# Kernel tuning notes

Hardware: AMD Instinct MI355X
Metric: run time of the kernel (lower is better)

The kernel has to match this reference:

```python
import jax, jax.numpy as jnp
import numpy as np

B, S, D, H = 4, 2048, 1024, 16
HD = D // H  # 64


def setup_inputs() -> dict:
    key = jax.random.key(0)
    k1, k2, k3 = jax.random.split(key, 3)
    scale = 1.0 / np.sqrt(D)
    return {
        "x": jax.random.normal(k1, (B, S, D), dtype=jnp.float32),
        "W_qkv": jax.random.normal(k2, (3 * D, D), dtype=jnp.float32) * scale,
        "b_qkv": jnp.zeros((3 * D,), dtype=jnp.float32),
        "W_out": jax.random.normal(k3, (D, D), dtype=jnp.float32) * scale,
        "b_out": jnp.zeros((D,), dtype=jnp.float32),
    }


def reference(x, W_qkv, b_qkv, W_out, b_out):
    b, s, d = x.shape
    # fused QKV projection: [b, s, 3d]
    qkv = jnp.einsum("bsd,ed->bse", x, W_qkv) + b_qkv
    # [b, s, H, 3*hd] -> [b, H, s, 3*hd]
    qkv = qkv.reshape(b, s, H, 3 * HD).transpose(0, 2, 1, 3)
    q, k, v = jnp.split(qkv, 3, axis=-1)  # each [b, H, s, hd]
    scaled = jnp.einsum("bhqd,bhkd->bhqk", q, k) / jnp.sqrt(jnp.float32(HD))
    attention = jax.nn.softmax(scaled, axis=-1)  # [b, H, s, s]
    values = jnp.einsum("bhqk,bhkd->bhqd", attention, v)
    values = values.transpose(0, 2, 1, 3).reshape(b, s, d)
    out = jnp.einsum("bsd,ed->bse", values, W_out) + b_out
    return out
```

## Files before the change

### kernel.cpp

```cpp
#include <hip/hip_runtime.h>

#define SEQ   2048
#define DM    1024
#define NHEAD 16
#define NBAT  4
#define NQKV  3072
#define MTOT  8192

typedef __attribute__((ext_vector_type(8))) short bf16x8;
typedef __attribute__((ext_vector_type(4))) float f32x4;
typedef __attribute__((ext_vector_type(16))) float f32x16;

__device__ __forceinline__ unsigned short f2bf(float f) {
    union { float f; unsigned int u; } v; v.f = f;
    return (unsigned short)((v.u + 0x7FFFu + ((v.u >> 16) & 1u)) >> 16);
}

__device__ __forceinline__ void gl_lds16(const void* g, void* l) {
    __builtin_amdgcn_global_load_lds(
        (const __attribute__((address_space(1))) unsigned int*)(unsigned long long)g,
        (__attribute__((address_space(3))) unsigned int*)(unsigned int)(unsigned long long)l,
        16, 0, 0);
}

__global__ __launch_bounds__(256) void k_cvt(const float* __restrict__ src,
                                             unsigned short* __restrict__ dst, int n4) {
    int i = blockIdx.x * blockDim.x + threadIdx.x;
    if (i >= n4) return;
    float4 v = reinterpret_cast<const float4*>(src)[i];
    ushort4 o = { f2bf(v.x), f2bf(v.y), f2bf(v.z), f2bf(v.w) };
    reinterpret_cast<ushort4*>(dst)[i] = o;
}

__global__ __launch_bounds__(256) void k_qkv(const unsigned short* __restrict__ X,
                                             const unsigned short* __restrict__ W,
                                             const float* __restrict__ bias,
                                             unsigned short* __restrict__ Qb,
                                             unsigned short* __restrict__ Kb,
                                             unsigned short* __restrict__ Vtb) {
    __shared__ short As[2][128 * 32];
    __shared__ short Bs[2][128 * 32];

    const int tid = threadIdx.x;
    const int lane = tid & 63;
    const int wid = tid >> 6;
    const int lr = lane & 15, g = lane >> 4;
    const int bm = blockIdx.x / (NQKV / 128);
    const int bn = blockIdx.x % (NQKV / 128);
    const int m0 = bm * 128, n0 = bn * 128;
    const int wr = (wid >> 1) * 64, wc = (wid & 1) * 64;

    const f32x4 fz = {0.f, 0.f, 0.f, 0.f};
    f32x4 acc[4][4];
#pragma unroll
    for (int i = 0; i < 4; ++i)
#pragma unroll
        for (int j = 0; j < 4; ++j) acc[i][j] = fz;

    auto stage = [&](int buf, int kt) {
#pragma unroll
        for (int p = 0; p < 2; ++p) {
            int c = wid * 128 + p * 64 + lane;
            int r_ = c >> 2;
            int kc = (c & 3) ^ (r_ & 3);
            gl_lds16(X + (size_t)(m0 + r_) * DM + kt * 32 + kc * 8, &As[buf][c * 8]);
            gl_lds16(W + (size_t)(n0 + r_) * DM + kt * 32 + kc * 8, &Bs[buf][c * 8]);
        }
    };

    stage(0, 0);
    __syncthreads();

    for (int kt = 0; kt < 32; ++kt) {
        const int cur = kt & 1;
        if (kt + 1 < 32) stage(cur ^ 1, kt + 1);
        bf16x8 a[4], b[4];
#pragma unroll
        for (int i = 0; i < 4; ++i) {
            int ra = wr + i * 16 + lr;
            a[i] = *(const bf16x8*)&As[cur][ra * 32 + ((g ^ (ra & 3)) * 8)];
            int rb = wc + i * 16 + lr;
            b[i] = *(const bf16x8*)&Bs[cur][rb * 32 + ((g ^ (rb & 3)) * 8)];
        }
#pragma unroll
        for (int i = 0; i < 4; ++i)
#pragma unroll
            for (int j = 0; j < 4; ++j)
                acc[i][j] = __builtin_amdgcn_mfma_f32_16x16x32_bf16(a[i], b[j], acc[i][j], 0, 0, 0);
        __syncthreads();
    }

#pragma unroll
    for (int j = 0; j < 4; ++j) {
        const int col = n0 + wc + j * 16 + lr;
        const int h = col / 192;
        const int cc = col - h * 192;
        const int part = cc >> 6;
        const int hd = cc & 63;
        const float bv = bias[col];
#pragma unroll
        for (int i = 0; i < 4; ++i) {
            const int mbase = m0 + wr + i * 16 + g * 4;
            const int b_ = mbase >> 11;
            const int s_ = mbase & 2047;
            const int bh = b_ * NHEAD + h;
            if (part == 2) {
                ushort4 pk = { f2bf(acc[i][j][0] + bv), f2bf(acc[i][j][1] + bv),
                               f2bf(acc[i][j][2] + bv), f2bf(acc[i][j][3] + bv) };
                *(ushort4*)&Vtb[((size_t)bh * 64 + hd) * SEQ + s_] = pk;
            } else {
#pragma unroll
                for (int r = 0; r < 4; ++r) {
                    const size_t idx = ((size_t)bh * SEQ + s_ + r) * 64 + hd;
                    float v = acc[i][j][r] + bv;
                    if (part == 0) Qb[idx] = f2bf(v * (0.125f * 1.44269504f));
                    else           Kb[idx] = f2bf(v);
                }
            }
        }
    }
}

__global__ __launch_bounds__(256) void k_attn(const unsigned short* __restrict__ Qb,
                                              const unsigned short* __restrict__ Kb,
                                              const unsigned short* __restrict__ Vtb,
                                              unsigned short* __restrict__ Ob) {
    __shared__ short Ks[2][64 * 64];
    __shared__ short Vs[2][64 * 64];

    const int tid = threadIdx.x;
    const int lane = tid & 63;
    const int wid = tid >> 6;
    const int bh = blockIdx.x >> 4;
    const int qt = blockIdx.x & 15;
    const int c = lane & 31;
    const int hi = lane >> 5;

    const unsigned short* Qh = Qb + (size_t)bh * SEQ * 64;
    const unsigned short* Kh = Kb + (size_t)bh * SEQ * 64;
    const unsigned short* Vh = Vtb + (size_t)bh * 64 * SEQ;

    const int q0 = qt * 128 + wid * 32;

    bf16x8 qf[4];
#pragma unroll
    for (int kc = 0; kc < 4; ++kc)
        qf[kc] = *(const bf16x8*)&Qh[(size_t)(q0 + c) * 64 + kc * 16 + hi * 8];

    f32x16 oacc[2];
    f32x16 lacc;
    f32x16 fz16;
#pragma unroll
    for (int r = 0; r < 16; ++r) { oacc[0][r] = 0.f; oacc[1][r] = 0.f; lacc[r] = 0.f; fz16[r] = 0.f; }

    auto stageK = [&](int buf, int kt) {
#pragma unroll
        for (int p = 0; p < 2; ++p) {
            int ci = wid * 128 + p * 64 + lane;
            int r_ = ci >> 3;
            int kc = (ci & 7) ^ (r_ & 7);
            gl_lds16(Kh + (size_t)(kt * 64 + r_) * 64 + kc * 8, &Ks[buf][ci * 8]);
        }
    };
    auto stageV = [&](int buf, int kt) {
#pragma unroll
        for (int p = 0; p < 2; ++p) {
            int ci = wid * 128 + p * 64 + lane;
            int r_ = ci >> 3;
            int kc = (ci & 7) ^ (r_ & 7);
            gl_lds16(Vh + (size_t)r_ * SEQ + kt * 64 + kc * 8, &Vs[buf][ci * 8]);
        }
    };

    stageK(0, 0);
    stageV(0, 0);
    __syncthreads();

    auto tile = [&](int cur, int kt) {
        if (kt + 1 < 32) { stageK(cur ^ 1, kt + 1); stageV(cur ^ 1, kt + 1); }

        f32x16 st[2];
        __builtin_amdgcn_s_setprio(1);
#pragma unroll
        for (int t = 0; t < 2; ++t) {
            const int row = t * 32 + c;
            bf16x8 kf0 = *(const bf16x8*)&Ks[cur][row * 64 + (((hi) ^ (row & 7)) * 8)];
            st[t] = __builtin_amdgcn_mfma_f32_32x32x16_bf16(kf0, qf[0], fz16, 0, 0, 0);
#pragma unroll
            for (int kc = 1; kc < 4; ++kc) {
                bf16x8 kf = *(const bf16x8*)&Ks[cur][row * 64 + (((kc * 2 + hi) ^ (row & 7)) * 8)];
                st[t] = __builtin_amdgcn_mfma_f32_32x32x16_bf16(kf, qf[kc], st[t], 0, 0, 0);
            }
        }
        __builtin_amdgcn_s_setprio(0);

#pragma unroll
        for (int t = 0; t < 2; ++t)
#pragma unroll
            for (int r = 0; r < 16; ++r)
                st[t][r] = __builtin_amdgcn_exp2f(st[t][r]);
#pragma unroll
        for (int r = 0; r < 16; ++r)
            lacc[r] += st[0][r] + st[1][r];

        bf16x8 pa[4];
#pragma unroll
        for (int t = 0; t < 2; ++t) {
            unsigned int qd[8];
#pragma unroll
            for (int i = 0; i < 8; ++i) {
                float lo = st[t][2 * i], hg = st[t][2 * i + 1];
                unsigned int d;
                asm("v_cvt_pk_bf16_f32 %0, %1, %2" : "=v"(d) : "v"(lo), "v"(hg));
                qd[i] = d;
            }
            union { unsigned int u[4]; bf16x8 v; } pk0, pk1;
            {
                unsigned int f0 = hi ? qd[0] : qd[2];
                unsigned int g0 = (unsigned int)__shfl_xor((int)f0, 32);
                pk0.u[0] = hi ? g0 : qd[0];
                pk0.u[2] = hi ? qd[2] : g0;
                unsigned int f1 = hi ? qd[1] : qd[3];
                unsigned int g1 = (unsigned int)__shfl_xor((int)f1, 32);
                pk0.u[1] = hi ? g1 : qd[1];
                pk0.u[3] = hi ? qd[3] : g1;
            }
            {
                unsigned int f0 = hi ? qd[4] : qd[6];
                unsigned int g0 = (unsigned int)__shfl_xor((int)f0, 32);
                pk1.u[0] = hi ? g0 : qd[4];
                pk1.u[2] = hi ? qd[6] : g0;
                unsigned int f1 = hi ? qd[5] : qd[7];
                unsigned int g1 = (unsigned int)__shfl_xor((int)f1, 32);
                pk1.u[1] = hi ? g1 : qd[5];
                pk1.u[3] = hi ? qd[7] : g1;
            }
            pa[t * 2] = pk0.v;
            pa[t * 2 + 1] = pk1.v;
        }

        __builtin_amdgcn_s_setprio(1);
#pragma unroll
        for (int nb = 0; nb < 2; ++nb) {
            const int row = nb * 32 + c;
#pragma unroll
            for (int ks = 0; ks < 4; ++ks) {
                bf16x8 vf = *(const bf16x8*)&Vs[cur][row * 64 + (((ks * 2 + hi) ^ (row & 7)) * 8)];
                oacc[nb] = __builtin_amdgcn_mfma_f32_32x32x16_bf16(pa[ks], vf, oacc[nb], 0, 0, 0);
            }
        }
        __builtin_amdgcn_s_setprio(0);

        __syncthreads();
    };

    for (int kt = 0; kt < 32; kt += 2) { tile(0, kt); tile(1, kt + 1); }

    float lred[16];
#pragma unroll
    for (int r = 0; r < 16; ++r) lred[r] = lacc[r];
#pragma unroll
    for (int s2 = 8; s2 > 0; s2 >>= 1)
#pragma unroll
        for (int r = 0; r < s2; ++r) lred[r] += lred[r + s2];
    const float l_all = lred[0] + __shfl_xor(lred[0], 32);

    const int b_ = bh >> 4, h_ = bh & 15;
    const float linv = 1.0f / l_all;
#pragma unroll
    for (int r = 0; r < 16; ++r) {
        const int qrow = (r & 3) + 8 * (r >> 2) + 4 * hi;
        const float fr = __shfl(linv, qrow);
        const size_t mrow = (size_t)b_ * SEQ + q0 + qrow;
#pragma unroll
        for (int nb = 0; nb < 2; ++nb)
            Ob[mrow * DM + h_ * 64 + nb * 32 + c] = f2bf(oacc[nb][r] * fr);
    }
}

__global__ __launch_bounds__(256) void k_out(const unsigned short* __restrict__ A,
                                             const unsigned short* __restrict__ W,
                                             const float* __restrict__ bias,
                                             float* __restrict__ O) {
    __shared__ short As[2][128 * 32];
    __shared__ short Bs[2][128 * 32];

    const int tid = threadIdx.x;
    const int lane = tid & 63;
    const int wid = tid >> 6;
    const int lr = lane & 15, g = lane >> 4;
    const int bm = blockIdx.x / (DM / 128);
    const int bn = blockIdx.x % (DM / 128);
    const int m0 = bm * 128, n0 = bn * 128;
    const int wr = (wid >> 1) * 64, wc = (wid & 1) * 64;

    const f32x4 fz = {0.f, 0.f, 0.f, 0.f};
    f32x4 acc[4][4];
#pragma unroll
    for (int i = 0; i < 4; ++i)
#pragma unroll
        for (int j = 0; j < 4; ++j) acc[i][j] = fz;

    auto stage = [&](int buf, int kt) {
#pragma unroll
        for (int p = 0; p < 2; ++p) {
            int c = wid * 128 + p * 64 + lane;
            int r_ = c >> 2;
            int kc = (c & 3) ^ (r_ & 3);
            gl_lds16(A + (size_t)(m0 + r_) * DM + kt * 32 + kc * 8, &As[buf][c * 8]);
            gl_lds16(W + (size_t)(n0 + r_) * DM + kt * 32 + kc * 8, &Bs[buf][c * 8]);
        }
    };

    stage(0, 0);
    __syncthreads();

    for (int kt = 0; kt < 32; ++kt) {
        const int cur = kt & 1;
        if (kt + 1 < 32) stage(cur ^ 1, kt + 1);
        bf16x8 a[4], b[4];
#pragma unroll
        for (int i = 0; i < 4; ++i) {
            int ra = wr + i * 16 + lr;
            a[i] = *(const bf16x8*)&As[cur][ra * 32 + ((g ^ (ra & 3)) * 8)];
            int rb = wc + i * 16 + lr;
            b[i] = *(const bf16x8*)&Bs[cur][rb * 32 + ((g ^ (rb & 3)) * 8)];
        }
#pragma unroll
        for (int i = 0; i < 4; ++i)
#pragma unroll
            for (int j = 0; j < 4; ++j)
                acc[i][j] = __builtin_amdgcn_mfma_f32_16x16x32_bf16(a[i], b[j], acc[i][j], 0, 0, 0);
        __syncthreads();
    }

#pragma unroll
    for (int j = 0; j < 4; ++j) {
        const int col = n0 + wc + j * 16 + lr;
        const float bv = bias[col];
#pragma unroll
        for (int i = 0; i < 4; ++i) {
            const int mb = m0 + wr + i * 16 + g * 4;
#pragma unroll
            for (int r = 0; r < 4; ++r)
                O[(size_t)(mb + r) * DM + col] = acc[i][j][r] + bv;
        }
    }
}

extern "C" void kernel_launch(void* const* d_in, const int* in_sizes, int n_in,
                              void* d_out, int out_size, void* d_ws, size_t ws_size,
                              hipStream_t stream) {
    const float* x    = (const float*)d_in[0];
    const float* Wqkv = (const float*)d_in[1];
    const float* bqkv = (const float*)d_in[2];
    const float* Wout = (const float*)d_in[3];
    const float* bout = (const float*)d_in[4];
    float* out = (float*)d_out;

    char* ws = (char*)d_ws;
    unsigned short* xb   = (unsigned short*)(ws);
    unsigned short* wqb  = (unsigned short*)(ws + (16u << 20));
    unsigned short* wob  = (unsigned short*)(ws + (22u << 20));
    unsigned short* Qb   = (unsigned short*)(ws + (24u << 20));
    unsigned short* Kb   = (unsigned short*)(ws + (40u << 20));
    unsigned short* Vtb  = (unsigned short*)(ws + (56u << 20));
    unsigned short* valb = (unsigned short*)(ws + (72u << 20));

    k_cvt<<<8192, 256, 0, stream>>>(x, xb, 2097152);
    k_cvt<<<3072, 256, 0, stream>>>(Wqkv, wqb, 786432);
    k_cvt<<<1024, 256, 0, stream>>>(Wout, wob, 262144);
    k_qkv<<<64 * 24, 256, 0, stream>>>(xb, wqb, bqkv, Qb, Kb, Vtb);
    k_attn<<<64 * 16, 256, 0, stream>>>(Qb, Kb, Vtb, valb);
    k_out<<<64 * 8, 256, 0, stream>>>(valb, wob, bout, out);
}
```

Before: 215.3 us.

## Fuse conversion kernels, remap blocks per XCD, use permlane32 swap

Merges the three fp32-to-bf16 conversion launches into one kernel, which removes two launch gaps. Remaps block indices in the QKV, attention and output kernels so that consecutive logical tiles land on the same XCD (blockIdx & 7 striding), aiming for better L2 locality of shared operands. Replaces the shuffle-plus-select exchange of P fragments in attention with permlane32_swap instructions, cutting cross-lane ops. The swap semantics must match the old shuffle pattern exactly, otherwise P is packed wrongly.

New measurement: 202.4 us. 1.06x faster.

```diff
diff --git a/kernel.cpp b/kernel.cpp
--- a/kernel.cpp
+++ b/kernel.cpp
@@ -10,6 +10,7 @@
 typedef __attribute__((ext_vector_type(8))) short bf16x8;
 typedef __attribute__((ext_vector_type(4))) float f32x4;
 typedef __attribute__((ext_vector_type(16))) float f32x16;
+typedef __attribute__((ext_vector_type(2))) unsigned int uint2v;
 
 __device__ __forceinline__ unsigned short f2bf(float f) {
     union { float f; unsigned int u; } v; v.f = f;
@@ -23,13 +24,20 @@
         16, 0, 0);
 }
 
-__global__ __launch_bounds__(256) void k_cvt(const float* __restrict__ src,
-                                             unsigned short* __restrict__ dst, int n4) {
-    int i = blockIdx.x * blockDim.x + threadIdx.x;
-    if (i >= n4) return;
-    float4 v = reinterpret_cast<const float4*>(src)[i];
+__global__ __launch_bounds__(256) void k_cvt_all(const float* __restrict__ x,
+                                                 const float* __restrict__ wq,
+                                                 const float* __restrict__ wo,
+                                                 unsigned short* __restrict__ xb,
+                                                 unsigned short* __restrict__ wqb,
+                                                 unsigned short* __restrict__ wob) {
+    int i = blockIdx.x * 256 + threadIdx.x;
+    const float* s; unsigned short* d; int j;
+    if (i < 2097152)      { s = x;  d = xb;  j = i; }
+    else if (i < 2883584) { s = wq; d = wqb; j = i - 2097152; }
+    else                  { s = wo; d = wob; j = i - 2883584; }
+    float4 v = reinterpret_cast<const float4*>(s)[j];
     ushort4 o = { f2bf(v.x), f2bf(v.y), f2bf(v.z), f2bf(v.w) };
-    reinterpret_cast<ushort4*>(dst)[i] = o;
+    reinterpret_cast<ushort4*>(d)[j] = o;
 }
 
 __global__ __launch_bounds__(256) void k_qkv(const unsigned short* __restrict__ X,
@@ -45,8 +53,9 @@
     const int lane = tid & 63;
     const int wid = tid >> 6;
     const int lr = lane & 15, g = lane >> 4;
-    const int bm = blockIdx.x / (NQKV / 128);
-    const int bn = blockIdx.x % (NQKV / 128);
+    const int lb = (blockIdx.x & 7) * 192 + (blockIdx.x >> 3);
+    const int bm = lb / (NQKV / 128);
+    const int bn = lb % (NQKV / 128);
     const int m0 = bm * 128, n0 = bn * 128;
     const int wr = (wid >> 1) * 64, wc = (wid & 1) * 64;
 
@@ -131,8 +140,9 @@
     const int tid = threadIdx.x;
     const int lane = tid & 63;
     const int wid = tid >> 6;
-    const int bh = blockIdx.x >> 4;
-    const int qt = blockIdx.x & 15;
+    const int lb = (blockIdx.x & 7) * 128 + (blockIdx.x >> 3);
+    const int bh = lb >> 4;
+    const int qt = lb & 15;
     const int c = lane & 31;
     const int hi = lane >> 5;
 
@@ -214,27 +224,13 @@
                 asm("v_cvt_pk_bf16_f32 %0, %1, %2" : "=v"(d) : "v"(lo), "v"(hg));
                 qd[i] = d;
             }
+            uint2v s02 = __builtin_amdgcn_permlane32_swap(qd[0], qd[2], false, false);
+            uint2v s13 = __builtin_amdgcn_permlane32_swap(qd[1], qd[3], false, false);
+            uint2v s46 = __builtin_amdgcn_permlane32_swap(qd[4], qd[6], false, false);
+            uint2v s57 = __builtin_amdgcn_permlane32_swap(qd[5], qd[7], false, false);
             union { unsigned int u[4]; bf16x8 v; } pk0, pk1;
-            {
-                unsigned int f0 = hi ? qd[0] : qd[2];
-                unsigned int g0 = (unsigned int)__shfl_xor((int)f0, 32);
-                pk0.u[0] = hi ? g0 : qd[0];
-                pk0.u[2] = hi ? qd[2] : g0;
-                unsigned int f1 = hi ? qd[1] : qd[3];
-                unsigned int g1 = (unsigned int)__shfl_xor((int)f1, 32);
-                pk0.u[1] = hi ? g1 : qd[1];
-                pk0.u[3] = hi ? qd[3] : g1;
-            }
-            {
-                unsigned int f0 = hi ? qd[4] : qd[6];
-                unsigned int g0 = (unsigned int)__shfl_xor((int)f0, 32);
-                pk1.u[0] = hi ? g0 : qd[4];
-                pk1.u[2] = hi ? qd[6] : g0;
-                unsigned int f1 = hi ? qd[5] : qd[7];
-                unsigned int g1 = (unsigned int)__shfl_xor((int)f1, 32);
-                pk1.u[1] = hi ? g1 : qd[5];
-                pk1.u[3] = hi ? qd[7] : g1;
-            }
+            pk0.u[0] = s02.x; pk0.u[1] = s13.x; pk0.u[2] = s02.y; pk0.u[3] = s13.y;
+            pk1.u[0] = s46.x; pk1.u[1] = s57.x; pk1.u[2] = s46.y; pk1.u[3] = s57.y;
             pa[t * 2] = pk0.v;
             pa[t * 2 + 1] = pk1.v;
         }
@@ -289,8 +285,9 @@
     const int lane = tid & 63;
     const int wid = tid >> 6;
     const int lr = lane & 15, g = lane >> 4;
-    const int bm = blockIdx.x / (DM / 128);
-    const int bn = blockIdx.x % (DM / 128);
+    const int lb = (blockIdx.x & 7) * 64 + (blockIdx.x >> 3);
+    const int bm = lb / (DM / 128);
+    const int bn = lb % (DM / 128);
     const int m0 = bm * 128, n0 = bn * 128;
     const int wr = (wid >> 1) * 64, wc = (wid & 1) * 64;
 
@@ -367,9 +364,7 @@
     unsigned short* Vtb  = (unsigned short*)(ws + (56u << 20));
     unsigned short* valb = (unsigned short*)(ws + (72u << 20));
 
-    k_cvt<<<8192, 256, 0, stream>>>(x, xb, 2097152);
-    k_cvt<<<3072, 256, 0, stream>>>(Wqkv, wqb, 786432);
-    k_cvt<<<1024, 256, 0, stream>>>(Wout, wob, 262144);
+    k_cvt_all<<<12288, 256, 0, stream>>>(x, Wqkv, Wout, xb, wqb, wob);
     k_qkv<<<64 * 24, 256, 0, stream>>>(xb, wqb, bqkv, Qb, Kb, Vtb);
     k_attn<<<64 * 16, 256, 0, stream>>>(Qb, Kb, Vtb, valb);
     k_out<<<64 * 8, 256, 0, stream>>>(valb, wob, bout, out);
```
